# Optimization experiments

Measured on AMD Instinct MI355X. Metric: run time of the kernel, lower is better.

## Reference

```python
import math
import jax, jax.numpy as jnp
import numpy as np

B, L, IN_DIM, D, OUT_DIM = 4, 4096, 512, 64, 512


def setup_inputs() -> dict:
    key = jax.random.key(0)
    ks = jax.random.split(key, 9)
    s_in = 1.0 / math.sqrt(IN_DIM)
    s_d = 1.0 / math.sqrt(D)
    return {
        "x": jax.random.normal(ks[0], (B, L, IN_DIM), jnp.float32),
        "Wq": jax.random.normal(ks[1], (IN_DIM, D), jnp.float32) * s_in,
        "bq": jax.random.normal(ks[2], (D,), jnp.float32) * s_in,
        "Wk": jax.random.normal(ks[3], (IN_DIM, D), jnp.float32) * s_in,
        "bk": jax.random.normal(ks[4], (D,), jnp.float32) * s_in,
        "Wv": jax.random.normal(ks[5], (IN_DIM, D), jnp.float32) * s_in,
        "bv": jax.random.normal(ks[6], (D,), jnp.float32) * s_in,
        "Wo": jax.random.normal(ks[7], (D, OUT_DIM), jnp.float32) * s_d,
        "bo": jax.random.normal(ks[8], (OUT_DIM,), jnp.float32) * s_d,
    }


def reference(x, Wq, bq, Wk, bk, Wv, bv, Wo, bo):
    # q, k, v: [B, L, D]
    q = x @ Wq + bq
    k = x @ Wk + bk
    v = x @ Wv + bv
    scale = 1.0 / math.sqrt(D)
    # scores: [B, Lq, Lk]
    scores = jnp.einsum("bqd,bkd->bqk", q, k) * scale
    # NOTE: original uses nn.Softmax(dim=1) -> softmax over the QUERY axis (axis=1)
    attention = jax.nn.softmax(scores, axis=1)
    values_with_attention = jnp.einsum("bqk,bkd->bqd", attention, v)
    output = values_with_attention @ Wo + bo
    return (output, attention)
```

## Files before the change

### kernel.cpp

```cpp
#include <hip/hip_runtime.h>
#include <hip/hip_fp16.h>
#include <math.h>

#define Bdim 4
#define Lseq 4096
#define INDIM 512
#define DH 64
#define OUTD 512
#define SCALE 0.125f
#define KSPL 8
#define QSPL 8
#define BL (Bdim * Lseq)

typedef _Float16 f16;
typedef _Float16 h8 __attribute__((ext_vector_type(8)));
typedef float f4 __attribute__((ext_vector_type(4)));
typedef float f2 __attribute__((ext_vector_type(2)));

#define MFMA(a, b, c) __builtin_amdgcn_mfma_f32_16x16x32_f16(a, b, c, 0, 0, 0)

__global__ __launch_bounds__(512) void proj_qkv(const float* __restrict__ x,
                                                const float* __restrict__ Wq,
                                                const float* __restrict__ bq,
                                                const float* __restrict__ Wk,
                                                const float* __restrict__ bk,
                                                const float* __restrict__ Wv,
                                                const float* __restrict__ bv,
                                                f16* __restrict__ qh,
                                                f16* __restrict__ kh,
                                                f16* __restrict__ vt) {
    __shared__ float xT[64 * 68];
    __shared__ float Ws[3][64 * 68];
    int t = threadIdx.x;
    int row0 = blockIdx.x * 64;
    int r2 = t >> 4, c4 = t & 15;
    float acc[3][2][4] = {};
    for (int kc = 0; kc < INDIM; kc += 64) {
        __syncthreads();
        {
            int row = t >> 3, kq = (t & 7) * 8;
            const float4* src = (const float4*)(x + (size_t)(row0 + row) * INDIM + kc + kq);
            float tmp[8];
#pragma unroll
            for (int i = 0; i < 2; ++i) {
                float4 v = src[i];
                tmp[4*i+0] = v.x; tmp[4*i+1] = v.y; tmp[4*i+2] = v.z; tmp[4*i+3] = v.w;
            }
#pragma unroll
            for (int j = 0; j < 8; ++j) xT[(kq + j) * 68 + row] = tmp[j];
        }
        {
            int k = t >> 3, dq = (t & 7) * 8;
            const float4* sq = (const float4*)(Wq + (size_t)(kc + k) * DH + dq);
            const float4* sk = (const float4*)(Wk + (size_t)(kc + k) * DH + dq);
            const float4* sv = (const float4*)(Wv + (size_t)(kc + k) * DH + dq);
#pragma unroll
            for (int i = 0; i < 2; ++i) {
                *(float4*)(&Ws[0][k * 68 + dq + 4 * i]) = sq[i];
                *(float4*)(&Ws[1][k * 68 + dq + 4 * i]) = sk[i];
                *(float4*)(&Ws[2][k * 68 + dq + 4 * i]) = sv[i];
            }
        }
        __syncthreads();
#pragma unroll 4
        for (int k = 0; k < 64; ++k) {
            f2 xv = *(f2*)(xT + k * 68 + r2 * 2);
            f4 w0 = *(f4*)(&Ws[0][k * 68 + c4 * 4]);
            f4 w1 = *(f4*)(&Ws[1][k * 68 + c4 * 4]);
            f4 w2 = *(f4*)(&Ws[2][k * 68 + c4 * 4]);
#pragma unroll
            for (int i = 0; i < 2; ++i)
#pragma unroll
                for (int j = 0; j < 4; ++j) {
                    acc[0][i][j] += xv[i] * w0[j];
                    acc[1][i][j] += xv[i] * w1[j];
                    acc[2][i][j] += xv[i] * w2[j];
                }
        }
    }
#pragma unroll
    for (int i = 0; i < 2; ++i) {
        size_t row = row0 + r2 * 2 + i;
#pragma unroll
        for (int j = 0; j < 4; ++j) {
            int d = c4 * 4 + j;
            qh[row * DH + d] = (f16)((acc[0][i][j] + bq[d]) * SCALE);
            kh[row * DH + d] = (f16)(acc[1][i][j] + bk[d]);
        }
    }
    __syncthreads();
#pragma unroll
    for (int i = 0; i < 2; ++i)
#pragma unroll
        for (int j = 0; j < 4; ++j)
            xT[(c4 * 4 + j) * 68 + r2 * 2 + i] = acc[2][i][j] + bv[c4 * 4 + j];
    __syncthreads();
    {
        int b = row0 >> 12;
        int krow = row0 & (Lseq - 1);
        int d = t >> 3, kq = (t & 7) * 8;
        h8 pack;
#pragma unroll
        for (int j = 0; j < 8; ++j) pack[j] = (f16)xT[d * 68 + kq + j];
        *(h8*)(vt + ((size_t)b * DH + d) * Lseq + krow + kq) = pack;
    }
}

__global__ __launch_bounds__(256) void col_stats(const f16* __restrict__ qh,
                                                 const f16* __restrict__ kh,
                                                 float* __restrict__ lsum) {
    __shared__ __align__(16) f16 qlds[2][64 * 72];
    int t = threadIdx.x;
    int w = t >> 6, lane = t & 63;
    int l15 = lane & 15, quad = lane >> 4;
    int b = blockIdx.y;
    int kblk = blockIdx.x * 128;
    int qbase = blockIdx.z * (Lseq / QSPL);

    h8 a[2][2];
#pragma unroll
    for (int kt = 0; kt < 2; ++kt) {
        const h8* kr = (const h8*)(kh + ((size_t)b * Lseq + kblk + w * 32 + kt * 16 + l15) * DH + quad * 8);
        a[kt][0] = kr[0];
        a[kt][1] = kr[4];
    }
    float lp[2][4] = {};

#pragma unroll
    for (int i = 0; i < 2; ++i) {
        int lin = i * 256 + t;
        int row = lin >> 3, c8 = lin & 7;
        *(h8*)(qlds[0] + row * 72 + c8 * 8) =
            *(const h8*)(qh + ((size_t)b * Lseq + qbase + row) * DH + c8 * 8);
    }
    __syncthreads();

    for (int it = 0; it < (Lseq / QSPL) / 64; ++it) {
        h8 s0, s1;
        int r0_ = 0, c0_ = 0, r1_ = 0, c1_ = 0;
        if (it < 7) {
            int lin0 = t, lin1 = 256 + t;
            r0_ = lin0 >> 3; c0_ = lin0 & 7;
            r1_ = lin1 >> 3; c1_ = lin1 & 7;
            s0 = *(const h8*)(qh + ((size_t)b * Lseq + qbase + (it + 1) * 64 + r0_) * DH + c0_ * 8);
            s1 = *(const h8*)(qh + ((size_t)b * Lseq + qbase + (it + 1) * 64 + r1_) * DH + c1_ * 8);
        }
        const f16* qb = qlds[it & 1];
#pragma unroll
        for (int nt = 0; nt < 4; ++nt) {
            const f16* qp = qb + (nt * 16 + l15) * 72 + quad * 8;
            h8 b0 = *(const h8*)qp;
            h8 b1 = *(const h8*)(qp + 32);
#pragma unroll
            for (int kt = 0; kt < 2; ++kt) {
                f4 c = {0.f, 0.f, 0.f, 0.f};
                c = MFMA(a[kt][0], b0, c);
                c = MFMA(a[kt][1], b1, c);
#pragma unroll
                for (int reg = 0; reg < 4; ++reg) lp[kt][reg] += __expf(c[reg]);
            }
        }
        if (it < 7) {
            f16* qn = qlds[(it & 1) ^ 1];
            *(h8*)(qn + r0_ * 72 + c0_ * 8) = s0;
            *(h8*)(qn + r1_ * 72 + c1_ * 8) = s1;
        }
        __syncthreads();
    }
#pragma unroll
    for (int kt = 0; kt < 2; ++kt)
#pragma unroll
        for (int reg = 0; reg < 4; ++reg) {
            float v = lp[kt][reg];
            v += __shfl_xor(v, 1);
            v += __shfl_xor(v, 2);
            v += __shfl_xor(v, 4);
            v += __shfl_xor(v, 8);
            if (l15 == 0)
                atomicAdd(&lsum[(size_t)b * Lseq + kblk + w * 32 + kt * 16 + quad * 4 + reg], v);
        }
}

__global__ __launch_bounds__(256, 4) void attn_pv(const f16* __restrict__ qh,
                                                  const f16* __restrict__ kh,
                                                  const f16* __restrict__ vt,
                                                  const float* __restrict__ lsum,
                                                  float* __restrict__ att,
                                                  f16* __restrict__ opart) {
    __shared__ __align__(16) f16 klds[2][64 * 72];
    __shared__ __align__(16) f16 es[4][32 * 80];
    int t = threadIdx.x;
    int w = t >> 6, lane = t & 63;
    int l15 = lane & 15, quad = lane >> 4;
    int b = blockIdx.y;
    int q0 = blockIdx.x * 128 + w * 32;
    int split = blockIdx.z;
    int kstart = split * (Lseq / KSPL);

    h8 aq[2][2];
#pragma unroll
    for (int mt = 0; mt < 2; ++mt) {
        const h8* qp = (const h8*)(qh + ((size_t)b * Lseq + q0 + mt * 16 + l15) * DH + quad * 8);
        aq[mt][0] = qp[0];
        aq[mt][1] = qp[4];
    }
    f4 o[2][4];
#pragma unroll
    for (int mt = 0; mt < 2; ++mt)
#pragma unroll
        for (int nt = 0; nt < 4; ++nt) o[mt][nt] = (f4){0.f, 0.f, 0.f, 0.f};

    const float* lsb = lsum + (size_t)b * Lseq;
    f16* ew = es[w];

#pragma unroll
    for (int i = 0; i < 2; ++i) {
        int lin = i * 256 + t;
        int row = lin >> 3, c8 = lin & 7;
        *(h8*)(klds[0] + row * 72 + c8 * 8) =
            *(const h8*)(kh + ((size_t)b * Lseq + kstart + row) * DH + c8 * 8);
    }
    __syncthreads();

    for (int it = 0; it < 8; ++it) {
        int kbase = kstart + it * 64;
        const f16* kb = klds[it & 1];

        h8 s0, s1;
        int r0_ = 0, c0_ = 0, r1_ = 0, c1_ = 0;
        if (it < 7) {
            int lin0 = t, lin1 = 256 + t;
            r0_ = lin0 >> 3; c0_ = lin0 & 7;
            r1_ = lin1 >> 3; c1_ = lin1 & 7;
            s0 = *(const h8*)(kh + ((size_t)b * Lseq + kbase + 64 + r0_) * DH + c0_ * 8);
            s1 = *(const h8*)(kh + ((size_t)b * Lseq + kbase + 64 + r1_) * DH + c1_ * 8);
        }

#pragma unroll
        for (int nt = 0; nt < 4; ++nt) {
            const f16* kp = kb + (nt * 16 + l15) * 72 + quad * 8;
            h8 b0 = *(const h8*)kp;
            h8 b1 = *(const h8*)(kp + 32);
            float rlv = 1.0f / lsb[kbase + nt * 16 + l15];
#pragma unroll
            for (int mt = 0; mt < 2; ++mt) {
                f4 c = {0.f, 0.f, 0.f, 0.f};
                c = MFMA(aq[mt][0], b0, c);
                c = MFMA(aq[mt][1], b1, c);
#pragma unroll
                for (int reg = 0; reg < 4; ++reg)
                    ew[(mt * 16 + quad * 4 + reg) * 80 + nt * 16 + l15] =
                        (f16)(__expf(c[reg]) * rlv);
            }
        }

        {
            int g = lane >> 3, c8 = lane & 7;
#pragma unroll
            for (int rr = 0; rr < 4; ++rr) {
                int row = rr * 8 + g;
                h8 hv = *(const h8*)(ew + row * 80 + c8 * 8);
                f4 v0, v1;
#pragma unroll
                for (int j = 0; j < 4; ++j) {
                    v0[j] = (float)hv[j];
                    v1[j] = (float)hv[4 + j];
                }
                float* dst = att + ((size_t)b * Lseq + q0 + row) * Lseq + kbase + c8 * 8;
                *(f4*)dst = v0;
                *(f4*)(dst + 4) = v1;
            }
        }

        h8 ae[2][2];
#pragma unroll
        for (int mt = 0; mt < 2; ++mt) {
            const f16* ep = ew + (mt * 16 + l15) * 80 + quad * 8;
            ae[mt][0] = *(const h8*)ep;
            ae[mt][1] = *(const h8*)(ep + 32);
        }
#pragma unroll
        for (int nt = 0; nt < 4; ++nt) {
            const h8* vp = (const h8*)(vt + ((size_t)b * DH + nt * 16 + l15) * Lseq + kbase + quad * 8);
            h8 bv0 = vp[0];
            h8 bv1 = vp[4];
            o[0][nt] = MFMA(ae[0][0], bv0, o[0][nt]);
            o[0][nt] = MFMA(ae[0][1], bv1, o[0][nt]);
            o[1][nt] = MFMA(ae[1][0], bv0, o[1][nt]);
            o[1][nt] = MFMA(ae[1][1], bv1, o[1][nt]);
        }

        if (it < 7) {
            f16* kn = klds[(it & 1) ^ 1];
            *(h8*)(kn + r0_ * 72 + c0_ * 8) = s0;
            *(h8*)(kn + r1_ * 72 + c1_ * 8) = s1;
        }
        __syncthreads();
    }

#pragma unroll
    for (int mt = 0; mt < 2; ++mt)
#pragma unroll
        for (int nt = 0; nt < 4; ++nt)
#pragma unroll
            for (int reg = 0; reg < 4; ++reg) {
                size_t qrow = (size_t)b * Lseq + q0 + mt * 16 + quad * 4 + reg;
                opart[((size_t)split * BL + qrow) * DH + nt * 16 + l15] = (f16)o[mt][nt][reg];
            }
}

#define WOFF(c) ((c) * 8 + ((c) >> 2) * 4)

__global__ __launch_bounds__(256) void out_proj(const f16* __restrict__ opart,
                                                const float* __restrict__ Wo,
                                                const float* __restrict__ bo,
                                                float* __restrict__ out) {
    __shared__ float osT[64 * 68];
    __shared__ float wos[64 * 144];
    int t = threadIdx.x;
    int rg = blockIdx.x, oq = blockIdx.y;
#pragma unroll
    for (int j = 0; j < 8; ++j) {
        int idx = j * 256 + t;
        int dd = idx >> 5, c4b = idx & 31;
        int c8b = c4b >> 1, half = (c4b & 1) * 4;
        *(float4*)(wos + dd * 144 + WOFF(c8b) + half) =
            *(const float4*)(Wo + (size_t)dd * OUTD + oq * 128 + c4b * 4);
    }
    {
        int row = t >> 2, dq = (t & 3) * 16;
        float s[16] = {};
#pragma unroll
        for (int sp = 0; sp < KSPL; ++sp) {
            const h8* src = (const h8*)(opart + ((size_t)sp * BL + (size_t)rg * 64 + row) * DH + dq);
            h8 v0 = src[0], v1 = src[1];
#pragma unroll
            for (int jj = 0; jj < 8; ++jj) {
                s[jj] += (float)v0[jj];
                s[8 + jj] += (float)v1[jj];
            }
        }
#pragma unroll
        for (int jj = 0; jj < 16; ++jj) osT[(dq + jj) * 68 + row] = s[jj];
    }
    __syncthreads();
    int r4 = t >> 4, c8 = t & 15;
    float acc[4][8] = {};
#pragma unroll 8
    for (int dd = 0; dd < DH; ++dd) {
        f4 ov = *(f4*)(osT + dd * 68 + r4 * 4);
        f4 w0 = *(f4*)(wos + dd * 144 + WOFF(c8));
        f4 w1 = *(f4*)(wos + dd * 144 + WOFF(c8) + 4);
#pragma unroll
        for (int i = 0; i < 4; ++i)
#pragma unroll
            for (int j = 0; j < 4; ++j) {
                acc[i][j]     += ov[i] * w0[j];
                acc[i][4 + j] += ov[i] * w1[j];
            }
    }
    f4 b0 = *(const f4*)(bo + oq * 128 + c8 * 8);
    f4 b1 = *(const f4*)(bo + oq * 128 + c8 * 8 + 4);
#pragma unroll
    for (int i = 0; i < 4; ++i) {
        size_t row = (size_t)rg * 64 + r4 * 4 + i;
        f4 r0, r1;
#pragma unroll
        for (int j = 0; j < 4; ++j) {
            r0[j] = acc[i][j] + b0[j];
            r1[j] = acc[i][4 + j] + b1[j];
        }
        *(f4*)(out + row * OUTD + oq * 128 + c8 * 8) = r0;
        *(f4*)(out + row * OUTD + oq * 128 + c8 * 8 + 4) = r1;
    }
}

extern "C" void kernel_launch(void* const* d_in, const int* in_sizes, int n_in,
                              void* d_out, int out_size, void* d_ws, size_t ws_size,
                              hipStream_t stream) {
    const float* x  = (const float*)d_in[0];
    const float* Wq = (const float*)d_in[1];
    const float* bq = (const float*)d_in[2];
    const float* Wk = (const float*)d_in[3];
    const float* bk = (const float*)d_in[4];
    const float* Wv = (const float*)d_in[5];
    const float* bv = (const float*)d_in[6];
    const float* Wo = (const float*)d_in[7];
    const float* bo = (const float*)d_in[8];

    float* out = (float*)d_out;
    float* att = out + (size_t)BL * OUTD;

    char* ws = (char*)d_ws;
    f16*   qh    = (f16*)(ws + 0);
    f16*   kh    = (f16*)(ws + (size_t)(2 << 20));
    f16*   vt    = (f16*)(ws + (size_t)(4 << 20));
    float* lsum  = (float*)(ws + (size_t)(6 << 20));
    f16*   opart = (f16*)(ws + (size_t)(7 << 20));

    hipMemsetAsync(lsum, 0, (size_t)BL * sizeof(float), stream);
    proj_qkv<<<dim3(BL / 64), 512, 0, stream>>>(x, Wq, bq, Wk, bk, Wv, bv, qh, kh, vt);
    col_stats<<<dim3(Lseq / 128, Bdim, QSPL), 256, 0, stream>>>(qh, kh, lsum);
    attn_pv<<<dim3(Lseq / 128, Bdim, KSPL), 256, 0, stream>>>(qh, kh, vt, lsum, att, opart);
    out_proj<<<dim3(BL / 64, OUTD / 128), 256, 0, stream>>>(opart, Wo, bo, out);
}
```

Before: 452.5 us.

## Move QKV projection to split-fp16 MFMA with pretransposed hi/lo weights

Replaces the scalar FP32 FMA QKV projection with MFMA 16x16x32 f16 instructions. fp32 accuracy is emulated with a hi/lo split, using three products per pair (hi*hi, lo*hi, hi*lo). A new small kernel transposes Wq/Wk/Wv and splits them into fp16 hi and lo parts in workspace. The projection register-prefetches the next x and weight tile while the MFMAs run on the current one. This adds a kernel launch and some extra LDS, and loses a little precision compared with true fp32.

```diff
diff --git a/kernel.cpp b/kernel.cpp
--- a/kernel.cpp
+++ b/kernel.cpp
@@ -14,96 +14,170 @@
 
 typedef _Float16 f16;
 typedef _Float16 h8 __attribute__((ext_vector_type(8)));
+typedef _Float16 h4 __attribute__((ext_vector_type(4)));
 typedef float f4 __attribute__((ext_vector_type(4)));
-typedef float f2 __attribute__((ext_vector_type(2)));
 
 #define MFMA(a, b, c) __builtin_amdgcn_mfma_f32_16x16x32_f16(a, b, c, 0, 0, 0)
 
-__global__ __launch_bounds__(512) void proj_qkv(const float* __restrict__ x,
-                                                const float* __restrict__ Wq,
+__global__ __launch_bounds__(256) void wtrans(const float* __restrict__ Wq,
+                                              const float* __restrict__ Wk,
+                                              const float* __restrict__ Wv,
+                                              f16* __restrict__ whi,
+                                              f16* __restrict__ wlo) {
+    __shared__ float tile[64 * 68];
+    int t = threadIdx.x;
+    int kt = blockIdx.x * 64;
+    const float* W = (blockIdx.y == 0) ? Wq : (blockIdx.y == 1) ? Wk : Wv;
+    {
+        int r = t >> 2, c4 = (t & 3) * 16;
+        const float4* src = (const float4*)(W + (size_t)(kt + r) * DH + c4);
+#pragma unroll
+        for (int i = 0; i < 4; ++i)
+            *(float4*)(tile + r * 68 + c4 + 4 * i) = src[i];
+    }
+    __syncthreads();
+    {
+        int d = t >> 2, k8 = (t & 3) * 16;
+        h8 hi0, hi1, lo0, lo1;
+#pragma unroll
+        for (int j = 0; j < 8; ++j) {
+            float v0 = tile[(k8 + j) * 68 + d];
+            float v1 = tile[(k8 + 8 + j) * 68 + d];
+            f16 h0 = (f16)v0, h1 = (f16)v1;
+            hi0[j] = h0; lo0[j] = (f16)(v0 - (float)h0);
+            hi1[j] = h1; lo1[j] = (f16)(v1 - (float)h1);
+        }
+        size_t base = ((size_t)blockIdx.y * DH + d) * INDIM + kt + k8;
+        *(h8*)(whi + base) = hi0;
+        *(h8*)(whi + base + 8) = hi1;
+        *(h8*)(wlo + base) = lo0;
+        *(h8*)(wlo + base + 8) = lo1;
+    }
+}
+
+__global__ __launch_bounds__(256) void proj_qkv(const float* __restrict__ x,
+                                                const f16* __restrict__ whi,
+                                                const f16* __restrict__ wlo,
                                                 const float* __restrict__ bq,
-                                                const float* __restrict__ Wk,
                                                 const float* __restrict__ bk,
-                                                const float* __restrict__ Wv,
                                                 const float* __restrict__ bv,
                                                 f16* __restrict__ qh,
                                                 f16* __restrict__ kh,
                                                 f16* __restrict__ vt) {
-    __shared__ float xT[64 * 68];
-    __shared__ float Ws[3][64 * 68];
+    __shared__ __align__(16) f16 xh[64 * 72];
+    __shared__ __align__(16) f16 xl[64 * 72];
+    __shared__ __align__(16) f16 wl[6][64 * 72];
     int t = threadIdx.x;
-    int row0 = blockIdx.x * 64;
-    int r2 = t >> 4, c4 = t & 15;
-    float acc[3][2][4] = {};
-    for (int kc = 0; kc < INDIM; kc += 64) {
+    int w = t >> 6, lane = t & 63;
+    int l15 = lane & 15, quad = lane >> 4;
+    size_t row0 = (size_t)blockIdx.x * 64;
+
+    int xr = t >> 2, xkq = (t & 3) * 16;
+    int wd = t >> 2, wko = (t & 3) * 16;
+
+    f4 acc[3][4];
+#pragma unroll
+    for (int m = 0; m < 3; ++m)
+#pragma unroll
+        for (int nt = 0; nt < 4; ++nt) acc[m][nt] = (f4){0.f, 0.f, 0.f, 0.f};
+
+    f4 xs[4];
+    h8 wsr[12];
+
+#define PROJ_ISSUE(kc)                                                             \
+    {                                                                              \
+        const f4* xsrc = (const f4*)(x + (row0 + xr) * INDIM + (kc) + xkq);        \
+        _Pragma("unroll") for (int i = 0; i < 4; ++i) xs[i] = xsrc[i];             \
+        _Pragma("unroll") for (int p = 0; p < 6; ++p) {                            \
+            const f16* src = ((p & 1) ? wlo : whi) +                               \
+                             ((size_t)(p >> 1) * DH + wd) * INDIM + (kc) + wko;    \
+            wsr[p * 2] = *(const h8*)src;                                          \
+            wsr[p * 2 + 1] = *(const h8*)(src + 8);                                \
+        }                                                                          \
+    }
+
+#define PROJ_COMMIT()                                                              \
+    {                                                                              \
+        h8 hi0, hi1, lo0, lo1;                                                     \
+        _Pragma("unroll") for (int j = 0; j < 4; ++j) {                            \
+            _Pragma("unroll") for (int i = 0; i < 2; ++i) {                        \
+                float v0 = xs[i][j + 0] , v1 = xs[i][j]; (void)v1;                 \
+            }                                                                      \
+        }                                                                          \
+        _Pragma("unroll") for (int j = 0; j < 8; ++j) {                            \
+            float v0 = ((const float*)xs)[j];                                      \
+            float v1 = ((const float*)xs)[8 + j];                                  \
+            f16 h0 = (f16)v0, h1 = (f16)v1;                                        \
+            hi0[j] = h0; lo0[j] = (f16)(v0 - (float)h0);                           \
+            hi1[j] = h1; lo1[j] = (f16)(v1 - (float)h1);                           \
+        }                                                                          \
+        *(h8*)(xh + xr * 72 + xkq) = hi0;                                          \
+        *(h8*)(xh + xr * 72 + xkq + 8) = hi1;                                      \
+        *(h8*)(xl + xr * 72 + xkq) = lo0;                                          \
+        *(h8*)(xl + xr * 72 + xkq + 8) = lo1;                                      \
+        _Pragma("unroll") for (int p = 0; p < 6; ++p) {                            \
+            *(h8*)(wl[p] + wd * 72 + wko) = wsr[p * 2];                            \
+            *(h8*)(wl[p] + wd * 72 + wko + 8) = wsr[p * 2 + 1];                    \
+        }                                                                          \
+    }
+
+    PROJ_ISSUE(0);
+    PROJ_COMMIT();
+    __syncthreads();
+
+    int arow = w * 16 + l15;
+    for (int it = 0; it < 8; ++it) {
+        if (it < 7) PROJ_ISSUE((it + 1) * 64);
+
+        h8 ah0 = *(const h8*)(xh + arow * 72 + quad * 8);
+        h8 ah1 = *(const h8*)(xh + arow * 72 + 32 + quad * 8);
+        h8 al0 = *(const h8*)(xl + arow * 72 + quad * 8);
+        h8 al1 = *(const h8*)(xl + arow * 72 + 32 + quad * 8);
+#pragma unroll
+        for (int m = 0; m < 3; ++m) {
+            const f16* bh = wl[m * 2];
+            const f16* bl = wl[m * 2 + 1];
+#pragma unroll
+            for (int nt = 0; nt < 4; ++nt) {
+                int d = nt * 16 + l15;
+                h8 bh0 = *(const h8*)(bh + d * 72 + quad * 8);
+                h8 bh1 = *(const h8*)(bh + d * 72 + 32 + quad * 8);
+                h8 bl0 = *(const h8*)(bl + d * 72 + quad * 8);
+                h8 bl1 = *(const h8*)(bl + d * 72 + 32 + quad * 8);
+                f4 c = acc[m][nt];
+                c = MFMA(ah0, bh0, c);
+                c = MFMA(ah1, bh1, c);
+                c = MFMA(al0, bh0, c);
+                c = MFMA(al1, bh1, c);
+                c = MFMA(ah0, bl0, c);
+                c = MFMA(ah1, bl1, c);
+                acc[m][nt] = c;
+            }
+        }
         __syncthreads();
-        {
-            int row = t >> 3, kq = (t & 7) * 8;
-            const float4* src = (const float4*)(x + (size_t)(row0 + row) * INDIM + kc + kq);
-            float tmp[8];
-#pragma unroll
-            for (int i = 0; i < 2; ++i) {
-                float4 v = src[i];
-                tmp[4*i+0] = v.x; tmp[4*i+1] = v.y; tmp[4*i+2] = v.z; tmp[4*i+3] = v.w;
-            }
-#pragma unroll
-            for (int j = 0; j < 8; ++j) xT[(kq + j) * 68 + row] = tmp[j];
-        }
-        {
-            int k = t >> 3, dq = (t & 7) * 8;
-            const float4* sq = (const float4*)(Wq + (size_t)(kc + k) * DH + dq);
-            const float4* sk = (const float4*)(Wk + (size_t)(kc + k) * DH + dq);
-            const float4* sv = (const float4*)(Wv + (size_t)(kc + k) * DH + dq);
-#pragma unroll
-            for (int i = 0; i < 2; ++i) {
-                *(float4*)(&Ws[0][k * 68 + dq + 4 * i]) = sq[i];
-                *(float4*)(&Ws[1][k * 68 + dq + 4 * i]) = sk[i];
-                *(float4*)(&Ws[2][k * 68 + dq + 4 * i]) = sv[i];
-            }
-        }
+        if (it < 7) PROJ_COMMIT();
         __syncthreads();
-#pragma unroll 4
-        for (int k = 0; k < 64; ++k) {
-            f2 xv = *(f2*)(xT + k * 68 + r2 * 2);
-            f4 w0 = *(f4*)(&Ws[0][k * 68 + c4 * 4]);
-            f4 w1 = *(f4*)(&Ws[1][k * 68 + c4 * 4]);
-            f4 w2 = *(f4*)(&Ws[2][k * 68 + c4 * 4]);
-#pragma unroll
-            for (int i = 0; i < 2; ++i)
-#pragma unroll
-                for (int j = 0; j < 4; ++j) {
-                    acc[0][i][j] += xv[i] * w0[j];
-                    acc[1][i][j] += xv[i] * w1[j];
-                    acc[2][i][j] += xv[i] * w2[j];
-                }
-        }
-    }
-#pragma unroll
-    for (int i = 0; i < 2; ++i) {
-        size_t row = row0 + r2 * 2 + i;
-#pragma unroll
-        for (int j = 0; j < 4; ++j) {
-            int d = c4 * 4 + j;
-            qh[row * DH + d] = (f16)((acc[0][i][j] + bq[d]) * SCALE);
-            kh[row * DH + d] = (f16)(acc[1][i][j] + bk[d]);
-        }
-    }
-    __syncthreads();
-#pragma unroll
-    for (int i = 0; i < 2; ++i)
-#pragma unroll
-        for (int j = 0; j < 4; ++j)
-            xT[(c4 * 4 + j) * 68 + r2 * 2 + i] = acc[2][i][j] + bv[c4 * 4 + j];
-    __syncthreads();
-    {
-        int b = row0 >> 12;
-        int krow = row0 & (Lseq - 1);
-        int d = t >> 3, kq = (t & 7) * 8;
-        h8 pack;
-#pragma unroll
-        for (int j = 0; j < 8; ++j) pack[j] = (f16)xT[d * 68 + kq + j];
-        *(h8*)(vt + ((size_t)b * DH + d) * Lseq + krow + kq) = pack;
-    }
+    }
+
+    int b = (int)(row0 >> 12);
+    int kr0 = ((int)row0 & (Lseq - 1)) + w * 16 + quad * 4;
+#pragma unroll
+    for (int nt = 0; nt < 4; ++nt) {
+        int d = nt * 16 + l15;
+        float bqv = bq[d], bkv = bk[d], bvv = bv[d];
+#pragma unroll
+        for (int reg = 0; reg < 4; ++reg) {
+            size_t r = row0 + w * 16 + quad * 4 + reg;
+            qh[r * DH + d] = (f16)((acc[0][nt][reg] + bqv) * SCALE);
+            kh[r * DH + d] = (f16)(acc[1][nt][reg] + bkv);
+        }
+        h4 pv;
+#pragma unroll
+        for (int reg = 0; reg < 4; ++reg) pv[reg] = (f16)(acc[2][nt][reg] + bvv);
+        *(h4*)(vt + ((size_t)b * DH + d) * Lseq + kr0) = pv;
+    }
+#undef PROJ_ISSUE
+#undef PROJ_COMMIT
 }
 
 __global__ __launch_bounds__(256) void col_stats(const f16* __restrict__ qh,
@@ -397,9 +471,12 @@
     f16*   vt    = (f16*)(ws + (size_t)(4 << 20));
     float* lsum  = (float*)(ws + (size_t)(6 << 20));
     f16*   opart = (f16*)(ws + (size_t)(7 << 20));
+    f16*   whi   = (f16*)(ws + (size_t)(23 << 20));
+    f16*   wlo   = (f16*)(ws + (size_t)(23 << 20) + (size_t)(192 << 10));
 
     hipMemsetAsync(lsum, 0, (size_t)BL * sizeof(float), stream);
-    proj_qkv<<<dim3(BL / 64), 512, 0, stream>>>(x, Wq, bq, Wk, bk, Wv, bv, qh, kh, vt);
+    wtrans<<<dim3(INDIM / 64, 3), 256, 0, stream>>>(Wq, Wk, Wv, whi, wlo);
+    proj_qkv<<<dim3(BL / 64), 256, 0, stream>>>(x, whi, wlo, bq, bk, bv, qh, kh, vt);
     col_stats<<<dim3(Lseq / 128, Bdim, QSPL), 256, 0, stream>>>(qh, kh, lsum);
     attn_pv<<<dim3(Lseq / 128, Bdim, KSPL), 256, 0, stream>>>(qh, kh, vt, lsum, att, opart);
     out_proj<<<dim3(BL / 64, OUTD / 128), 256, 0, stream>>>(opart, Wo, bo, out);
```

Result: faster. 424.2 us (-6.3%).
